# Kernel tuning notes

Hardware: AMD Instinct MI355X
Metric: run time of the kernel (lower is better)

Reference implementation:

```python
import jax, jax.numpy as jnp
import numpy as np

B, N, C_IN, C_OUT, K, D_EMB = 64, 2048, 64, 64, 3, 10

def setup_inputs() -> dict:
    key = jax.random.key(0)
    k1, k2, k3, k4 = jax.random.split(key, 4)
    x = jax.random.normal(k1, (B, N, C_IN), dtype=jnp.float32)
    node_embeddings = jax.random.normal(k2, (N, D_EMB), dtype=jnp.float32)
    weights_pool = jax.random.normal(k3, (D_EMB, K, C_IN, C_OUT), dtype=jnp.float32) * 0.1
    bias_pool = jax.random.normal(k4, (D_EMB, C_OUT), dtype=jnp.float32) * 0.1
    return {"x": x, "node_embeddings": node_embeddings,
            "weights_pool": weights_pool, "bias_pool": bias_pool, "cheb_k": K}

def reference(x, node_embeddings, weights_pool, bias_pool, cheb_k):
    n = node_embeddings.shape[0]
    # adaptive adjacency: softmax over rows of relu(E E^T)
    supports = jax.nn.softmax(jax.nn.relu(node_embeddings @ node_embeddings.T), axis=1)  # [N,N]
    support_set = [jnp.eye(n, dtype=x.dtype), supports]
    for _ in range(2, cheb_k):
        support_set.append(2.0 * supports @ support_set[-1] - support_set[-2])
    supports_k = jnp.stack(support_set, axis=0)                     # [K,N,N]
    # per-node weights/bias generated from embedding
    weights = jnp.einsum('nd,dkio->nkio', node_embeddings, weights_pool)  # [N,K,Ci,Co]
    bias = node_embeddings @ bias_pool                               # [N,Co]
    # graph conv: gather Chebyshev-filtered features then per-node grouped GEMM
    x_g = jnp.einsum('knm,bmc->bnkc', supports_k, x)                 # [B,N,K,Ci]
    out = jnp.einsum('bnki,nkio->bno', x_g, weights) + bias          # [B,N,Co]
    return out
```

## Files before the change

kernel.cpp:

```cpp
#include <hip/hip_runtime.h>

typedef __attribute__((ext_vector_type(8))) short short8;
typedef __attribute__((ext_vector_type(4))) float f32x4;
typedef __attribute__((ext_vector_type(4))) unsigned short us4;
typedef __attribute__((ext_vector_type(8))) unsigned short us8;

constexpr int Bb = 64, Nn = 2048, CI = 64, CO = 64, KK = 3, DE = 10;
constexpr int NW = Bb * CI;
constexpr int WPSZ = KK * CI * CO;

__device__ __forceinline__ unsigned short f2bf(float f) {
  unsigned u = __float_as_uint(f);
  u += 0x7fff + ((u >> 16) & 1);
  return (unsigned short)(u >> 16);
}
__device__ __forceinline__ float bf2f(unsigned short h) {
  return __uint_as_float(((unsigned)h) << 16);
}
__device__ __forceinline__ void gl2lds16(const void* g, void* l) {
  __builtin_amdgcn_global_load_lds(
      (const __attribute__((address_space(1))) void*)g,
      (__attribute__((address_space(3))) void*)l, 16, 0, 0);
}

__global__ __launch_bounds__(256) void prep_kernel(
    const float* __restrict__ E, unsigned short* __restrict__ S,
    const float* __restrict__ x, unsigned short* __restrict__ Xrow,
    unsigned short* __restrict__ XT, const float* __restrict__ Wp,
    unsigned short* __restrict__ Wpf) {
  __shared__ float sh[5376];
  const int bid = blockIdx.x, t = threadIdx.x;

  if (bid < 2048) {
    const int n = bid;
    const int lane = t & 63, wv = t >> 6;
    float emb[DE];
#pragma unroll
    for (int d = 0; d < DE; d++) emb[d] = E[n * DE + d];

    float v[8];
    for (int h = 0; h < 4; h++) {
      __syncthreads();
      const float* src = E + (size_t)(512 * DE) * h;
#pragma unroll
      for (int q = 0; q < 5; q++) {
        const int idx = t + q * 256;
        *(float4*)&sh[idx * 4] = *(const float4*)(src + idx * 4);
      }
      __syncthreads();
#pragma unroll
      for (int jj = 0; jj < 2; jj++) {
        const int lm = t + jj * 256;
        const float2* er = (const float2*)&sh[lm * 10];
        float dot = 0.f;
#pragma unroll
        for (int p = 0; p < 5; p++) {
          const float2 e2 = er[p];
          dot += emb[2 * p] * e2.x + emb[2 * p + 1] * e2.y;
        }
        v[h * 2 + jj] = fmaxf(dot, 0.f);
      }
    }

    float r = -1e30f;
#pragma unroll
    for (int j = 0; j < 8; j++) r = fmaxf(r, v[j]);
#pragma unroll
    for (int off = 32; off; off >>= 1) r = fmaxf(r, __shfl_xor(r, off));
    if (lane == 0) sh[5120 + wv] = r;
    __syncthreads();
    const float rowmax = fmaxf(fmaxf(sh[5120], sh[5121]), fmaxf(sh[5122], sh[5123]));

    float lsum = 0.f;
#pragma unroll
    for (int j = 0; j < 8; j++) { v[j] = __expf(v[j] - rowmax); lsum += v[j]; }
#pragma unroll
    for (int off = 32; off; off >>= 1) lsum += __shfl_xor(lsum, off);
    if (lane == 0) sh[5128 + wv] = lsum;
    __syncthreads();
    const float inv = 1.f / (sh[5128] + sh[5129] + sh[5130] + sh[5131]);
#pragma unroll
    for (int j = 0; j < 8; j++) S[(size_t)n * Nn + t + j * 256] = f2bf(v[j] * inv);
  } else if (bid < 4096) {
    const int id = bid - 2048;
    const int b = id & 63, n0 = (id >> 6) * 64;
    const int i4 = (t & 15) * 4;
#pragma unroll
    for (int j = 0; j < 4; j++) {
      const int r = j * 16 + (t >> 4);
      const float4 v =
          *(const float4*)(x + (size_t)b * (Nn * CI) + (size_t)(n0 + r) * CI + i4);
      us4 o; o.x = f2bf(v.x); o.y = f2bf(v.y); o.z = f2bf(v.z); o.w = f2bf(v.w);
      *(us4*)(Xrow + (size_t)(n0 + r) * NW + b * CI + i4) = o;
      sh[r * 65 + i4 + 0] = v.x; sh[r * 65 + i4 + 1] = v.y;
      sh[r * 65 + i4 + 2] = v.z; sh[r * 65 + i4 + 3] = v.w;
    }
    __syncthreads();
    const int i = t >> 2, c0 = (t & 3) * 16;
    us8 p0, p1;
#pragma unroll
    for (int j = 0; j < 8; j++) p0[j] = f2bf(sh[(c0 + j) * 65 + i]);
#pragma unroll
    for (int j = 0; j < 8; j++) p1[j] = f2bf(sh[(c0 + 8 + j) * 65 + i]);
    unsigned short* dst = XT + (size_t)(b * CI + i) * Nn + n0 + c0;
    *(us8*)(dst) = p0;
    *(us8*)(dst + 8) = p1;
  } else {
    const int e4 = ((bid - 4096) * 256 + t) * 4;
    const int d = e4 / WPSZ;
    const int r = e4 - d * WPSZ;
    const int c = r >> 12, io = r & 4095;
    float4 v = *(const float4*)(Wp + (size_t)d * WPSZ + c * 4096 + io);
    if (c == 0) {
      const float4 w2 = *(const float4*)(Wp + (size_t)d * WPSZ + 2 * 4096 + io);
      v.x -= w2.x; v.y -= w2.y; v.z -= w2.z; v.w -= w2.w;
    } else if (c == 2) {
      v.x *= 2.f; v.y *= 2.f; v.z *= 2.f; v.w *= 2.f;
    }
    us4 o; o.x = f2bf(v.x); o.y = f2bf(v.y); o.z = f2bf(v.z); o.w = f2bf(v.w);
    *(us4*)(Wpf + e4) = o;
  }
}

__global__ __launch_bounds__(256) void mfma_gemm(
    const unsigned short* __restrict__ A, const unsigned short* __restrict__ Bt,
    unsigned short* __restrict__ Crow, unsigned short* __restrict__ Ct, int mode) {
  __shared__ unsigned short sm[12288];
  unsigned short* As = sm;
  unsigned short* Bs = sm + 8192;
  const int t = threadIdx.x, lane = t & 63, wave = t >> 6;
  const int n0 = blockIdx.x * 64, m0 = blockIdx.y * 128;
  const int wm = (wave & 1) * 64, wn = (wave >> 1) * 32;
  const int lr = lane & 15, lq = lane >> 4;

  f32x4 acc[4][2] = {};
  const int srow = lane >> 3;
  const int schunk = (lane & 7) ^ srow;

  for (int k0 = 0; k0 < 2048; k0 += 64) {
    __syncthreads();
#pragma unroll
    for (int j = 0; j < 4; j++) {
      const int r0 = (wave * 4 + j) * 8;
      gl2lds16(A + (size_t)(m0 + r0 + srow) * 2048 + k0 + schunk * 8, As + r0 * 64);
    }
#pragma unroll
    for (int j = 0; j < 2; j++) {
      const int r0 = (wave * 2 + j) * 8;
      gl2lds16(Bt + (size_t)(n0 + r0 + srow) * 2048 + k0 + schunk * 8, Bs + r0 * 64);
    }
    __syncthreads();
#pragma unroll
    for (int ks = 0; ks < 2; ks++) {
      short8 af[4], bfr[2];
#pragma unroll
      for (int i = 0; i < 4; i++) {
        const int m = wm + i * 16 + lr;
        const int slot = (ks * 4 + lq) ^ (m & 7);
        af[i] = *(const short8*)(As + m * 64 + slot * 8);
      }
#pragma unroll
      for (int j = 0; j < 2; j++) {
        const int n = wn + j * 16 + lr;
        const int slot = (ks * 4 + lq) ^ (n & 7);
        bfr[j] = *(const short8*)(Bs + n * 64 + slot * 8);
      }
#pragma unroll
      for (int i = 0; i < 4; i++)
#pragma unroll
        for (int j = 0; j < 2; j++)
          acc[i][j] = __builtin_amdgcn_mfma_f32_16x16x32_bf16(af[i], bfr[j], acc[i][j], 0, 0, 0);
    }
  }

  __syncthreads();
#pragma unroll
  for (int i = 0; i < 4; i++) {
#pragma unroll
    for (int r = 0; r < 4; r++) {
      const int m = wm + i * 16 + lq * 4 + r;
      const int sw = (m & 7) ^ ((m >> 3) & 7);
#pragma unroll
      for (int j = 0; j < 2; j++) {
        const int n = wn + j * 16 + lr;
        sm[m * 64 + (((n >> 3) ^ sw) * 8) + (n & 7)] = f2bf(acc[i][j][r]);
      }
    }
  }
  __syncthreads();

  {
    const int rr = t >> 3, cc = (t & 7) * 8;
#pragma unroll
    for (int p = 0; p < 4; p++) {
      const int m = p * 32 + rr;
      const int slot = (cc >> 3) ^ (m & 7) ^ ((m >> 3) & 7);
      const us8 v = *(const us8*)(sm + m * 64 + slot * 8);
      *(us8*)(Crow + (size_t)(m0 + m) * NW + n0 + cc) = v;
    }
  }
  if (mode == 0) {
    const int mc = (t & 15) * 8;
#pragma unroll
    for (int p = 0; p < 4; p++) {
      const int n = p * 16 + (t >> 4);
      us8 v;
#pragma unroll
      for (int q = 0; q < 8; q++) {
        const int m = mc + q;
        v[q] = sm[m * 64 + (((n >> 3) ^ (m & 7) ^ ((m >> 3) & 7)) * 8) + (n & 7)];
      }
      *(us8*)(Ct + (size_t)(n0 + n) * 2048 + m0 + mc) = v;
    }
  }
}

__global__ __launch_bounds__(256) void out_kernel(
    const unsigned short* __restrict__ Xrow, const unsigned short* __restrict__ XG1,
    const unsigned short* __restrict__ Yr, const float* __restrict__ E,
    const unsigned short* __restrict__ Wpf, const float* __restrict__ bp,
    float* __restrict__ out) {
  __shared__ unsigned short Wt[KK * CO * 64];
  __shared__ unsigned short Al[KK * Bb * CI];
  __shared__ float biasl[CO];

  const int n = blockIdx.x, t = threadIdx.x, lane = t & 63, wave = t >> 6;

  const unsigned short* srcs[KK] = {Xrow + (size_t)n * NW, XG1 + (size_t)n * NW,
                                    Yr + (size_t)n * NW};
  const int srow = lane >> 3;
  const int schunk = (lane & 7) ^ srow;
#pragma unroll
  for (int j = 0; j < 6; j++) {
    const int r0 = (wave * 6 + j) * 8;
    const int c = r0 >> 6, b0 = r0 & 63;
    gl2lds16(srcs[c] + (b0 + srow) * 64 + schunk * 8, Al + r0 * 64);
  }

  float emb[DE];
#pragma unroll
  for (int d = 0; d < DE; d++) emb[d] = E[n * DE + d];

  const int o8 = (t & 7) * 8;
#pragma unroll
  for (int j = 0; j < 6; j++) {
    const int c = j >> 1;
    const int i = (j & 1) * 32 + (t >> 3);
    float w[8] = {};
#pragma unroll
    for (int d = 0; d < DE; d++) {
      const us8 wp = *(const us8*)(Wpf + (size_t)d * WPSZ + c * 4096 + i * 64 + o8);
#pragma unroll
      for (int q = 0; q < 8; q++) w[q] += emb[d] * bf2f(wp[q]);
    }
    const int chunk = i >> 3, ilo = i & 7;
#pragma unroll
    for (int q = 0; q < 8; q++) {
      const int o = o8 + q;
      Wt[(c * 64 + o) * 64 + ((chunk ^ (o & 7)) * 8) + ilo] = f2bf(w[q]);
    }
  }
  if (t < CO) {
    float bsum = 0.f;
#pragma unroll
    for (int d = 0; d < DE; d++) bsum += emb[d] * bp[d * CO + t];
    biasl[t] = bsum;
  }
  __syncthreads();

  const int lr = lane & 15, lq = lane >> 4;
  f32x4 acc[4] = {};
#pragma unroll
  for (int kt = 0; kt < 6; kt++) {
    const int c = kt >> 1;
    const int chunk = (kt & 1) * 4 + lq;
    const int o = wave * 16 + lr;
    const short8 bfrag =
        *(const short8*)(Wt + (c * 64 + o) * 64 + (chunk ^ (o & 7)) * 8);
#pragma unroll
    for (int mt = 0; mt < 4; mt++) {
      const int b = mt * 16 + lr;
      const short8 afrag =
          *(const short8*)(Al + (c * 64 + b) * 64 + (chunk ^ (b & 7)) * 8);
      acc[mt] = __builtin_amdgcn_mfma_f32_16x16x32_bf16(afrag, bfrag, acc[mt], 0, 0, 0);
    }
  }

  __syncthreads();
  float* F = (float*)Wt;
#pragma unroll
  for (int mt = 0; mt < 4; mt++)
#pragma unroll
    for (int r = 0; r < 4; r++)
      F[(mt * 16 + lq * 4 + r) * 68 + wave * 16 + lr] = acc[mt][r];
  __syncthreads();

  const int bo = t >> 4, o4 = (t & 15) * 4;
#pragma unroll
  for (int mt = 0; mt < 4; mt++) {
    const int b = mt * 16 + bo;
    float4 v = *(const float4*)&F[b * 68 + o4];
    v.x += biasl[o4 + 0]; v.y += biasl[o4 + 1];
    v.z += biasl[o4 + 2]; v.w += biasl[o4 + 3];
    *(float4*)(out + (size_t)b * (Nn * CO) + (size_t)n * CO + o4) = v;
  }
}

extern "C" void kernel_launch(void* const* d_in, const int* in_sizes, int n_in,
                              void* d_out, int out_size, void* d_ws,
                              size_t ws_size, hipStream_t stream) {
  const float* x  = (const float*)d_in[0];
  const float* E  = (const float*)d_in[1];
  const float* Wp = (const float*)d_in[2];
  const float* bp = (const float*)d_in[3];
  float* out = (float*)d_out;

  unsigned short* ws   = (unsigned short*)d_ws;
  unsigned short* Xrow = ws;
  unsigned short* XG1r = Xrow + (size_t)Nn * NW;
  unsigned short* Yr   = XG1r + (size_t)Nn * NW;
  unsigned short* S    = Yr   + (size_t)Nn * NW;
  unsigned short* XT   = S    + (size_t)Nn * Nn;
  unsigned short* XG1T = XT   + (size_t)NW * Nn;
  unsigned short* Wpf  = XG1T + (size_t)NW * Nn;

  prep_kernel<<<4216, 256, 0, stream>>>(E, S, x, Xrow, XT, Wp, Wpf);

  dim3 g(NW / 64, Nn / 128);
  mfma_gemm<<<g, 256, 0, stream>>>(S, XT,   XG1r, XG1T, 0);
  mfma_gemm<<<g, 256, 0, stream>>>(S, XG1T, Yr,   nullptr, 1);

  out_kernel<<<Nn, 256, 0, stream>>>(Xrow, XG1r, Yr, E, Wpf, bp, out);
}
```

Before: 207.4 us.

## Split softmax supports into dedicated kernel computing eight rows per block

Moves the adaptive-adjacency softmax out of the combined prep kernel into its own kernel. Each wave now handles two rows, so each staged chunk of node embeddings in shared memory is reused by eight rows instead of one. The reductions become wave-local shuffles with no cross-wave shared-memory steps. The cost is an extra kernel launch, more registers per thread, and a write pattern for S that is strided by lane rather than contiguous per thread.

```diff
diff --git a/kernel.cpp b/kernel.cpp
--- a/kernel.cpp
+++ b/kernel.cpp
@@ -23,67 +23,75 @@
       (__attribute__((address_space(3))) void*)l, 16, 0, 0);
 }
 
+__global__ __launch_bounds__(256) void supports_kernel(
+    const float* __restrict__ E, unsigned short* __restrict__ S) {
+  __shared__ float El[5120];
+  const int t = threadIdx.x, lane = t & 63, wv = t >> 6;
+  const int n0 = blockIdx.x * 8;
+
+  float emb[2][DE];
+#pragma unroll
+  for (int r = 0; r < 2; r++)
+#pragma unroll
+    for (int d = 0; d < DE; d++) emb[r][d] = E[(n0 + wv * 2 + r) * DE + d];
+
+  float v[2][32];
+  for (int h = 0; h < 4; h++) {
+    __syncthreads();
+#pragma unroll
+    for (int q = 0; q < 5; q++) {
+      const int idx = t + q * 256;
+      *(float4*)&El[idx * 4] = *(const float4*)(E + 5120 * h + idx * 4);
+    }
+    __syncthreads();
+#pragma unroll
+    for (int j = 0; j < 8; j++) {
+      const int ml = lane + j * 64;
+      const float2* er = (const float2*)&El[ml * 10];
+      const float2 e0 = er[0], e1 = er[1], e2 = er[2], e3 = er[3], e4 = er[4];
+#pragma unroll
+      for (int r = 0; r < 2; r++) {
+        const float dot =
+            emb[r][0] * e0.x + emb[r][1] * e0.y + emb[r][2] * e1.x +
+            emb[r][3] * e1.y + emb[r][4] * e2.x + emb[r][5] * e2.y +
+            emb[r][6] * e3.x + emb[r][7] * e3.y + emb[r][8] * e4.x +
+            emb[r][9] * e4.y;
+        v[r][h * 8 + j] = fmaxf(dot, 0.f);
+      }
+    }
+  }
+
+#pragma unroll
+  for (int r = 0; r < 2; r++) {
+    float mx = -1e30f;
+#pragma unroll
+    for (int j = 0; j < 32; j++) mx = fmaxf(mx, v[r][j]);
+#pragma unroll
+    for (int off = 32; off; off >>= 1) mx = fmaxf(mx, __shfl_xor(mx, off));
+    float sum = 0.f;
+#pragma unroll
+    for (int j = 0; j < 32; j++) { v[r][j] = __expf(v[r][j] - mx); sum += v[r][j]; }
+#pragma unroll
+    for (int off = 32; off; off >>= 1) sum += __shfl_xor(sum, off);
+    const float inv = 1.f / sum;
+    unsigned short* dst = S + (size_t)(n0 + wv * 2 + r) * Nn;
+#pragma unroll
+    for (int j = 0; j < 32; j++) {
+      const int col = (j >> 3) * 512 + (j & 7) * 64 + lane;
+      dst[col] = f2bf(v[r][j] * inv);
+    }
+  }
+}
+
 __global__ __launch_bounds__(256) void prep_kernel(
-    const float* __restrict__ E, unsigned short* __restrict__ S,
     const float* __restrict__ x, unsigned short* __restrict__ Xrow,
     unsigned short* __restrict__ XT, const float* __restrict__ Wp,
     unsigned short* __restrict__ Wpf) {
-  __shared__ float sh[5376];
+  __shared__ float sh[4160];
   const int bid = blockIdx.x, t = threadIdx.x;
 
   if (bid < 2048) {
-    const int n = bid;
-    const int lane = t & 63, wv = t >> 6;
-    float emb[DE];
-#pragma unroll
-    for (int d = 0; d < DE; d++) emb[d] = E[n * DE + d];
-
-    float v[8];
-    for (int h = 0; h < 4; h++) {
-      __syncthreads();
-      const float* src = E + (size_t)(512 * DE) * h;
-#pragma unroll
-      for (int q = 0; q < 5; q++) {
-        const int idx = t + q * 256;
-        *(float4*)&sh[idx * 4] = *(const float4*)(src + idx * 4);
-      }
-      __syncthreads();
-#pragma unroll
-      for (int jj = 0; jj < 2; jj++) {
-        const int lm = t + jj * 256;
-        const float2* er = (const float2*)&sh[lm * 10];
-        float dot = 0.f;
-#pragma unroll
-        for (int p = 0; p < 5; p++) {
-          const float2 e2 = er[p];
-          dot += emb[2 * p] * e2.x + emb[2 * p + 1] * e2.y;
-        }
-        v[h * 2 + jj] = fmaxf(dot, 0.f);
-      }
-    }
-
-    float r = -1e30f;
-#pragma unroll
-    for (int j = 0; j < 8; j++) r = fmaxf(r, v[j]);
-#pragma unroll
-    for (int off = 32; off; off >>= 1) r = fmaxf(r, __shfl_xor(r, off));
-    if (lane == 0) sh[5120 + wv] = r;
-    __syncthreads();
-    const float rowmax = fmaxf(fmaxf(sh[5120], sh[5121]), fmaxf(sh[5122], sh[5123]));
-
-    float lsum = 0.f;
-#pragma unroll
-    for (int j = 0; j < 8; j++) { v[j] = __expf(v[j] - rowmax); lsum += v[j]; }
-#pragma unroll
-    for (int off = 32; off; off >>= 1) lsum += __shfl_xor(lsum, off);
-    if (lane == 0) sh[5128 + wv] = lsum;
-    __syncthreads();
-    const float inv = 1.f / (sh[5128] + sh[5129] + sh[5130] + sh[5131]);
-#pragma unroll
-    for (int j = 0; j < 8; j++) S[(size_t)n * Nn + t + j * 256] = f2bf(v[j] * inv);
-  } else if (bid < 4096) {
-    const int id = bid - 2048;
-    const int b = id & 63, n0 = (id >> 6) * 64;
+    const int b = bid & 63, n0 = (bid >> 6) * 64;
     const int i4 = (t & 15) * 4;
 #pragma unroll
     for (int j = 0; j < 4; j++) {
@@ -106,7 +114,7 @@
     *(us8*)(dst) = p0;
     *(us8*)(dst + 8) = p1;
   } else {
-    const int e4 = ((bid - 4096) * 256 + t) * 4;
+    const int e4 = ((bid - 2048) * 256 + t) * 4;
     const int d = e4 / WPSZ;
     const int r = e4 - d * WPSZ;
     const int c = r >> 12, io = r & 4095;
@@ -324,7 +332,8 @@
   unsigned short* XG1T = XT   + (size_t)NW * Nn;
   unsigned short* Wpf  = XG1T + (size_t)NW * Nn;
 
-  prep_kernel<<<4216, 256, 0, stream>>>(E, S, x, Xrow, XT, Wp, Wpf);
+  supports_kernel<<<256, 256, 0, stream>>>(E, S);
+  prep_kernel<<<2168, 256, 0, stream>>>(x, Xrow, XT, Wp, Wpf);
 
   dim3 g(NW / 64, Nn / 128);
   mfma_gemm<<<g, 256, 0, stream>>>(S, XT,   XG1r, XG1T, 0);
```

Measured after the change: 219.5 us. 1.06x slower.
